# Performance work log

Measured on AMD Instinct MI355X. Metric: run time of the kernel, lower is better.

The kernel has to match this reference:

```python
import jax, jax.numpy as jnp
import numpy as np

NUM_HEADS = 4
EPS = 1e-5

def _proj(x, W, b):
    # 1x1x1 Conv3d == channel-wise linear: x [B,C,H,W,D], W [Cout,Cin], b [Cout]
    return jnp.einsum('oc,bchwd->bohwd', W, x) + b[None, :, None, None, None]

def setup_inputs() -> dict:
    key = jax.random.key(0)
    ks = jax.random.split(key, 12)
    B, C, H, W, D = 2, 128, 16, 16, 16
    s = 1.0 / np.sqrt(C)
    inp = {
        'query_features': jax.random.normal(ks[0], (B, C, H, W, D), jnp.float32),
        'key_value_features': jax.random.normal(ks[1], (B, C, H, W, D), jnp.float32),
        'Wq': jax.random.normal(ks[2], (C, C), jnp.float32) * s,
        'bq': jax.random.normal(ks[3], (C,), jnp.float32) * 0.01,
        'Wk': jax.random.normal(ks[4], (C, C), jnp.float32) * s,
        'bk': jax.random.normal(ks[5], (C,), jnp.float32) * 0.01,
        'Wv': jax.random.normal(ks[6], (C, C), jnp.float32) * s,
        'bv': jax.random.normal(ks[7], (C,), jnp.float32) * 0.01,
        'Wo': jax.random.normal(ks[8], (C, C), jnp.float32) * s,
        'bo': jax.random.normal(ks[9], (C,), jnp.float32) * 0.01,
    }
    return inp

def reference(query_features, key_value_features, Wq, bq, Wk, bk, Wv, bv, Wo, bo):
    B, C, H, W, D = query_features.shape
    hd = C // NUM_HEADS  # head_dim
    N = H * W * D
    Q = _proj(query_features, Wq, bq).reshape(B, NUM_HEADS, hd, N)
    K = _proj(key_value_features, Wk, bk).reshape(B, NUM_HEADS, hd, N)
    V = _proj(key_value_features, Wv, bv).reshape(B, NUM_HEADS, hd, N)
    scale = hd ** -0.5
    attn = jnp.einsum('bhdn,bhdm->bhnm', Q, K) * scale  # [B,h,N,N]
    attn = jax.nn.softmax(attn, axis=-1)
    out = jnp.einsum('bhnm,bhdm->bhdn', attn, V).reshape(B, C, H, W, D)
    out = _proj(out, Wo, bo)
    res = query_features + out
    # InstanceNorm3d (affine=False): normalize over spatial dims per (B,C)
    mu = jnp.mean(res, axis=(2, 3, 4), keepdims=True)
    var = jnp.var(res, axis=(2, 3, 4), keepdims=True)
    return (res - mu) * jax.lax.rsqrt(var + EPS)
```

## Files before the change

### kernel.cpp

```cpp
#include <hip/hip_runtime.h>
#include <hip/hip_bf16.h>

typedef unsigned short u16;
typedef unsigned int u32;
typedef __bf16 bf16_t;
typedef bf16_t bf16x8 __attribute__((ext_vector_type(8)));
typedef float f32x4 __attribute__((ext_vector_type(4)));

#define NTOT 4096
#define CCH 128
#define QSCL 0.25503486703f

__device__ __forceinline__ float bf2f(u16 x) {
    return __uint_as_float(((u32)x) << 16);
}
__device__ __forceinline__ u32 pkbf(float a, float b) {
    __hip_bfloat162 h = __float22bfloat162_rn(make_float2(a, b));
    u32 r; __builtin_memcpy(&r, &h, 4); return r;
}
__device__ __forceinline__ u16 f2bf(float a) {
    return (u16)(pkbf(a, a) & 0xffffu);
}

__global__ __launch_bounds__(256) void prep_kernel(
    const float* __restrict__ Wq, const float* __restrict__ Wk,
    const float* __restrict__ Wv, const float* __restrict__ Wo,
    const float* __restrict__ bq,
    u16* __restrict__ Wqb, u16* __restrict__ Wkb,
    u16* __restrict__ Wvb, u16* __restrict__ Wob,
    float* __restrict__ bqs)
{
    const int idx = blockIdx.x * 256 + threadIdx.x;
    const int m = idx >> 13;
    const int e = idx & 8191;
    const float* src = (m == 0) ? Wq : (m == 1) ? Wk : (m == 2) ? Wv : Wo;
    u32* dst = (u32*)((m == 0) ? Wqb : (m == 1) ? Wkb : (m == 2) ? Wvb : Wob);
    const float s = (m == 0) ? QSCL : 1.0f;
    float2 f = ((const float2*)src)[e];
    dst[e] = pkbf(f.x * s, f.y * s);
    if (idx < CCH) bqs[idx] = bq[idx] * QSCL;
}

__global__ __launch_bounds__(256, 4) void proj_kernel(
    const float* __restrict__ xq, const float* __restrict__ xkv,
    const u16* __restrict__ Wqb, const float* __restrict__ bqs,
    const u16* __restrict__ Wkb, const float* __restrict__ bk_,
    const u16* __restrict__ Wvb, const float* __restrict__ bv_,
    u16* __restrict__ Qt, u16* __restrict__ Kt, u16* __restrict__ Vn)
{
    const int nt = blockIdx.x, p = blockIdx.y, b = blockIdx.z;
    const float* X    = (p == 0) ? xq : xkv;
    const u16*   Wb   = (p == 0) ? Wqb : (p == 1) ? Wkb : Wvb;
    const float* bias = (p == 0) ? bqs : (p == 1) ? bk_ : bv_;
    const int n0 = nt * 64;
    const int tid = threadIdx.x;

    __shared__ u16 Xt[64 * 128];
    __shared__ u16 Wl[128 * 136];

    #pragma unroll
    for (int k = 0; k < 4; ++k) {
        int n = tid & 63;
        int c = (tid >> 6) + k * 4;
        float f[8];
        #pragma unroll
        for (int j = 0; j < 8; ++j)
            f[j] = X[((size_t)(b * CCH) + 8 * c + j) * NTOT + n0 + n];
        uint4 vv = {pkbf(f[0], f[1]), pkbf(f[2], f[3]), pkbf(f[4], f[5]), pkbf(f[6], f[7])};
        *(uint4*)(Xt + n * 128 + ((c ^ (n & 7)) * 8)) = vv;
    }
    #pragma unroll
    for (int k = 0; k < 8; ++k) {
        int id = tid + k * 256;
        int row = id >> 4;
        int off = (id & 15) * 8;
        *(uint4*)(Wl + row * 136 + off) = *(const uint4*)(Wb + row * 128 + off);
    }
    __syncthreads();

    const int wave = tid >> 6, lane = tid & 63;
    const int quad = lane >> 4, l16 = lane & 15;
    f32x4 acc[8];
    #pragma unroll
    for (int cf = 0; cf < 8; ++cf) acc[cf] = (f32x4){0.f, 0.f, 0.f, 0.f};

    #pragma unroll
    for (int kk = 0; kk < 4; ++kk) {
        bf16x8 bx = *(const bf16x8*)(Xt + (wave * 16 + l16) * 128 +
                                     (((kk * 4 + quad) ^ (l16 & 7)) * 8));
        #pragma unroll
        for (int cf = 0; cf < 8; ++cf) {
            bf16x8 aw = *(const bf16x8*)(Wl + (cf * 16 + l16) * 136 + kk * 32 + quad * 8);
            acc[cf] = __builtin_amdgcn_mfma_f32_16x16x32_bf16(aw, bx, acc[cf], 0, 0, 0);
        }
    }

    const int n = n0 + wave * 16 + l16;
    #pragma unroll
    for (int cf = 0; cf < 8; ++cf) {
        float4 b4 = *(const float4*)(bias + cf * 16 + quad * 4);
        float v0 = acc[cf][0] + b4.x;
        float v1 = acc[cf][1] + b4.y;
        float v2 = acc[cf][2] + b4.z;
        float v3 = acc[cf][3] + b4.w;
        if (p < 2) {
            const int h = cf >> 1;
            const int d0 = (cf & 1) * 16 + quad * 4;
            u16* dst = (p == 0 ? Qt : Kt) + ((size_t)(b * 4 + h) * NTOT + n) * 32 + d0;
            uint2 vv = {pkbf(v0, v1), pkbf(v2, v3)};
            *(uint2*)dst = vv;
        } else {
            int c = cf * 16 + quad * 4;
            u16* dst = Vn + (size_t)(b * CCH + c) * NTOT + n;
            dst[0 * NTOT] = f2bf(v0); dst[1 * NTOT] = f2bf(v1);
            dst[2 * NTOT] = f2bf(v2); dst[3 * NTOT] = f2bf(v3);
        }
    }
}

__global__ __launch_bounds__(256, 2) void flash_attn_kernel(
    const u16* __restrict__ Qt, const u16* __restrict__ Kt,
    const u16* __restrict__ Vn, u16* __restrict__ pO, float* __restrict__ pL)
{
    const int bh = blockIdx.z, kc = blockIdx.y;
    const int wave = threadIdx.x >> 6, lane = threadIdx.x & 63;
    const int q = lane >> 4, l16 = lane & 15;
    const int q0w = blockIdx.x * 256 + wave * 64;

    const u16* Qbh = Qt + (size_t)bh * NTOT * 32;
    const u16* Kbh = Kt + (size_t)bh * NTOT * 32;
    const u16* Vg  = Vn + ((size_t)((bh >> 2) * CCH + (bh & 3) * 32)) * NTOT;

    __shared__ u16 Kb[2][2048];
    __shared__ u16 Vb[2][2048];
    __shared__ u16 Pb[4][1024];

    const int kbase = kc * 1024;

    bf16x8 bq[4];
    #pragma unroll
    for (int g = 0; g < 4; ++g)
        bq[g] = *(const bf16x8*)(Qbh + (size_t)(q0w + g * 16 + l16) * 32 + q * 8);

    const size_t ksrc = (size_t)(wave * 16 + l16) * 32 + q * 8;
    const size_t vsrc = (size_t)((wave & 1) * 16 + l16) * NTOT + (wave >> 1) * 32 + q * 8;
    const int kv_dst = wave * 512 + lane * 8;

    uint4 kreg = *(const uint4*)(Kbh + (size_t)kbase * 32 + ksrc);
    uint4 vreg = *(const uint4*)(Vg + vsrc + kbase);
    *(uint4*)(&Kb[0][kv_dst]) = kreg;
    *(uint4*)(&Vb[0][kv_dst]) = vreg;
    __syncthreads();

    f32x4 o[4][2];
    #pragma unroll
    for (int g = 0; g < 4; ++g) {
        o[g][0] = (f32x4){0,0,0,0};
        o[g][1] = (f32x4){0,0,0,0};
    }
    const f32x4 zero = {0,0,0,0};
    float lp[4] = {0.f, 0.f, 0.f, 0.f};

    u16* pw = &Pb[wave][0];
    const int pwr = (q >> 1) * 128 + l16 * 8 + (q & 1) * 4;
    const int prd0 = 0 * 512 + lane * 8;
    const int prd1 = 1 * 512 + lane * 8;

    for (int it = 0; it < 16; ++it) {
        const int cur = it & 1;
        if (it < 15) {
            const int m1 = kbase + (it + 1) * 64;
            kreg = *(const uint4*)(Kbh + (size_t)m1 * 32 + ksrc);
            vreg = *(const uint4*)(Vg + vsrc + m1);
        }
        f32x4 s[4][4];
        #pragma unroll
        for (int t = 0; t < 4; ++t) {
            bf16x8 ak = *(const bf16x8*)(&Kb[cur][t * 512 + lane * 8]);
            #pragma unroll
            for (int g = 0; g < 4; ++g)
                s[g][t] = __builtin_amdgcn_mfma_f32_16x16x32_bf16(ak, bq[g], zero, 0, 0, 0);
        }
        bf16x8 av00 = *(const bf16x8*)(&Vb[cur][0 * 512 + lane * 8]);
        bf16x8 av01 = *(const bf16x8*)(&Vb[cur][1 * 512 + lane * 8]);
        bf16x8 av10 = *(const bf16x8*)(&Vb[cur][2 * 512 + lane * 8]);
        bf16x8 av11 = *(const bf16x8*)(&Vb[cur][3 * 512 + lane * 8]);
        #pragma unroll
        for (int g = 0; g < 4; ++g) {
            #pragma unroll
            for (int t = 0; t < 4; ++t) {
                float p0 = __builtin_amdgcn_exp2f(s[g][t][0]);
                float p1 = __builtin_amdgcn_exp2f(s[g][t][1]);
                float p2 = __builtin_amdgcn_exp2f(s[g][t][2]);
                float p3 = __builtin_amdgcn_exp2f(s[g][t][3]);
                lp[g] += (p0 + p1) + (p2 + p3);
                uint2 wv = {pkbf(p0, p1), pkbf(p2, p3)};
                *(uint2*)(pw + (t >> 1) * 512 + (t & 1) * 256 + pwr) = wv;
            }
            bf16x8 pb0 = *(const bf16x8*)(pw + prd0);
            bf16x8 pb1 = *(const bf16x8*)(pw + prd1);
            o[g][0] = __builtin_amdgcn_mfma_f32_16x16x32_bf16(av00, pb0, o[g][0], 0, 0, 0);
            o[g][1] = __builtin_amdgcn_mfma_f32_16x16x32_bf16(av01, pb0, o[g][1], 0, 0, 0);
            o[g][0] = __builtin_amdgcn_mfma_f32_16x16x32_bf16(av10, pb1, o[g][0], 0, 0, 0);
            o[g][1] = __builtin_amdgcn_mfma_f32_16x16x32_bf16(av11, pb1, o[g][1], 0, 0, 0);
        }
        if (it < 15) {
            const int nb = (it + 1) & 1;
            *(uint4*)(&Kb[nb][kv_dst]) = kreg;
            *(uint4*)(&Vb[nb][kv_dst]) = vreg;
        }
        __syncthreads();
    }

    #pragma unroll
    for (int g = 0; g < 4; ++g) {
        lp[g] += __shfl_xor(lp[g], 16);
        lp[g] += __shfl_xor(lp[g], 32);
        const size_t ob = ((size_t)(kc * 8 + bh) * NTOT + q0w + g * 16 + l16) * 32 + q * 4;
        uint2 w0 = {pkbf(o[g][0][0], o[g][0][1]), pkbf(o[g][0][2], o[g][0][3])};
        uint2 w1 = {pkbf(o[g][1][0], o[g][1][1]), pkbf(o[g][1][2], o[g][1][3])};
        *(uint2*)(pO + ob)      = w0;
        *(uint2*)(pO + ob + 16) = w1;
        if (q == 0)
            pL[(size_t)(kc * 8 + bh) * NTOT + q0w + g * 16 + l16] = lp[g];
    }
}

__global__ __launch_bounds__(256, 4) void outproj_kernel(
    const float* __restrict__ xq,
    const u16* __restrict__ pO, const float* __restrict__ pL,
    const u16* __restrict__ Wob, const float* __restrict__ bo,
    float* __restrict__ res, float* __restrict__ partS, float* __restrict__ partQ)
{
    const int nt = blockIdx.x, ct = blockIdx.y, b = blockIdx.z;
    const int n0 = nt * 64;
    const int tid = threadIdx.x;

    __shared__ u16 Xt[64 * 128];
    __shared__ u16 Wl[64 * 136];

    #pragma unroll
    for (int k = 0; k < 4; ++k) {
        int cid = tid + k * 256;
        int n = cid >> 4;
        int ch = cid & 15;
        int bh = b * 4 + (ch >> 2);
        int d0 = (ch & 3) * 8;
        float l = 0.f;
        float v[8];
        #pragma unroll
        for (int j = 0; j < 8; ++j) v[j] = 0.f;
        #pragma unroll
        for (int kcc = 0; kcc < 4; ++kcc) {
            const size_t nrow = (size_t)(kcc * 8 + bh) * NTOT + n0 + n;
            l += pL[nrow];
            uint4 u = *(const uint4*)(pO + nrow * 32 + d0);
            const u32 uu[4] = {u.x, u.y, u.z, u.w};
            #pragma unroll
            for (int j = 0; j < 4; ++j) {
                v[2 * j]     += bf2f((u16)(uu[j] & 0xffffu));
                v[2 * j + 1] += bf2f((u16)(uu[j] >> 16));
            }
        }
        const float inv = 1.0f / l;
        uint4 vv = {pkbf(v[0] * inv, v[1] * inv), pkbf(v[2] * inv, v[3] * inv),
                    pkbf(v[4] * inv, v[5] * inv), pkbf(v[6] * inv, v[7] * inv)};
        *(uint4*)(Xt + n * 128 + ((ch ^ (n & 7)) * 8)) = vv;
    }
    #pragma unroll
    for (int k = 0; k < 4; ++k) {
        int id = tid + k * 256;
        int row = id >> 4;
        int off = (id & 15) * 8;
        *(uint4*)(Wl + row * 136 + off) =
            *(const uint4*)(Wob + (size_t)(ct * 64 + row) * 128 + off);
    }
    __syncthreads();

    const int wave = tid >> 6, lane = tid & 63;
    const int quad = lane >> 4, l16 = lane & 15;
    f32x4 acc[4];
    #pragma unroll
    for (int cf = 0; cf < 4; ++cf) acc[cf] = (f32x4){0.f, 0.f, 0.f, 0.f};

    #pragma unroll
    for (int kk = 0; kk < 4; ++kk) {
        bf16x8 bx = *(const bf16x8*)(Xt + (wave * 16 + l16) * 128 +
                                     (((kk * 4 + quad) ^ (l16 & 7)) * 8));
        #pragma unroll
        for (int cf = 0; cf < 4; ++cf) {
            bf16x8 aw = *(const bf16x8*)(Wl + (cf * 16 + l16) * 136 + kk * 32 + quad * 8);
            acc[cf] = __builtin_amdgcn_mfma_f32_16x16x32_bf16(aw, bx, acc[cf], 0, 0, 0);
        }
    }

    const int n = n0 + wave * 16 + l16;
    const int tile = nt * 4 + wave;
    #pragma unroll
    for (int cf = 0; cf < 4; ++cf) {
        float4 b4 = *(const float4*)(bo + ct * 64 + cf * 16 + quad * 4);
        const float bb[4] = {b4.x, b4.y, b4.z, b4.w};
        float sv[4], qv[4];
        #pragma unroll
        for (int r = 0; r < 4; ++r) {
            int c = ct * 64 + cf * 16 + quad * 4 + r;
            float v = acc[cf][r] + bb[r] + xq[(size_t)(b * CCH + c) * NTOT + n];
            res[(size_t)(b * CCH + c) * NTOT + n] = v;
            sv[r] = v;
            qv[r] = v * v;
        }
        #pragma unroll
        for (int off = 1; off < 16; off <<= 1) {
            #pragma unroll
            for (int r = 0; r < 4; ++r) {
                sv[r] += __shfl_xor(sv[r], off);
                qv[r] += __shfl_xor(qv[r], off);
            }
        }
        if (l16 == 0) {
            #pragma unroll
            for (int r = 0; r < 4; ++r) {
                int c = ct * 64 + cf * 16 + quad * 4 + r;
                partS[(size_t)(b * CCH + c) * 256 + tile] = sv[r];
                partQ[(size_t)(b * CCH + c) * 256 + tile] = qv[r];
            }
        }
    }
}

__global__ __launch_bounds__(256) void norm_kernel(
    const float* __restrict__ res, const float* __restrict__ partS,
    const float* __restrict__ partQ, float* __restrict__ out)
{
    const int c = blockIdx.x, b = blockIdx.y;
    const int tid = threadIdx.x;
    const size_t row = (size_t)(b * CCH + c);
    __shared__ float rs[4], rq[4];
    float s = partS[row * 256 + tid];
    float q = partQ[row * 256 + tid];
    #pragma unroll
    for (int off = 1; off < 64; off <<= 1) {
        s += __shfl_xor(s, off);
        q += __shfl_xor(q, off);
    }
    const int wv = tid >> 6, ln = tid & 63;
    if (ln == 0) { rs[wv] = s; rq[wv] = q; }
    __syncthreads();
    float ts = rs[0] + rs[1] + rs[2] + rs[3];
    float tq = rq[0] + rq[1] + rq[2] + rq[3];
    float mu  = ts * (1.0f / 4096.0f);
    float var = tq * (1.0f / 4096.0f) - mu * mu;
    float inv = rsqrtf(var + 1e-5f);
    const size_t base = row * NTOT;
    #pragma unroll
    for (int j = 0; j < 4; ++j) {
        int n = tid * 4 + j * 1024;
        float4 v = *(const float4*)(res + base + n);
        float4 o;
        o.x = (v.x - mu) * inv; o.y = (v.y - mu) * inv;
        o.z = (v.z - mu) * inv; o.w = (v.w - mu) * inv;
        *(float4*)(out + base + n) = o;
    }
}

extern "C" void kernel_launch(void* const* d_in, const int* in_sizes, int n_in,
                              void* d_out, int out_size, void* d_ws, size_t ws_size,
                              hipStream_t stream)
{
    const float* xq  = (const float*)d_in[0];
    const float* xkv = (const float*)d_in[1];
    const float* Wq  = (const float*)d_in[2];
    const float* bq  = (const float*)d_in[3];
    const float* Wk  = (const float*)d_in[4];
    const float* bk  = (const float*)d_in[5];
    const float* Wv  = (const float*)d_in[6];
    const float* bv  = (const float*)d_in[7];
    const float* Wo  = (const float*)d_in[8];
    const float* bo  = (const float*)d_in[9];
    float* out = (float*)d_out;

    char* ws = (char*)d_ws;
    const size_t MB = (size_t)1 << 20;
    u16* Qt = (u16*)(ws + 0 * MB);
    u16* Kt = (u16*)(ws + 2 * MB);
    u16* Vn = (u16*)(ws + 4 * MB);
    u16* pO = (u16*)(ws + 6 * MB);
    float* pL = (float*)(ws + 14 * MB);
    u16* Wqb = (u16*)(ws + 15 * MB);
    u16* Wkb = Wqb + 16384;
    u16* Wvb = Wkb + 16384;
    u16* Wob = Wvb + 16384;
    float* bqs = (float*)(Wob + 16384);
    float* res   = (float*)(ws + 16 * MB);
    float* partS = (float*)(ws + 20 * MB);
    float* partQ = (float*)(ws + 20 * MB + 262144);

    prep_kernel<<<dim3(128), 256, 0, stream>>>(Wq, Wk, Wv, Wo, bq, Wqb, Wkb, Wvb, Wob, bqs);
    proj_kernel<<<dim3(64, 3, 2), 256, 0, stream>>>(xq, xkv, Wqb, bqs, Wkb, bk, Wvb, bv, Qt, Kt, Vn);
    flash_attn_kernel<<<dim3(16, 4, 8), 256, 0, stream>>>(Qt, Kt, Vn, pO, pL);
    outproj_kernel<<<dim3(64, 2, 2), 256, 0, stream>>>(xq, pO, pL, Wob, bo, res, partS, partQ);
    norm_kernel<<<dim3(128, 2), 256, 0, stream>>>(res, partS, partQ, out);
}
```

Measured before the change: 126.7 us.

## Fuse weight conversion into projections and double flash-attention key splits

```diff
diff --git a/kernel.cpp b/kernel.cpp
--- a/kernel.cpp
+++ b/kernel.cpp
@@ -22,36 +22,18 @@
     return (u16)(pkbf(a, a) & 0xffffu);
 }
 
-__global__ __launch_bounds__(256) void prep_kernel(
-    const float* __restrict__ Wq, const float* __restrict__ Wk,
-    const float* __restrict__ Wv, const float* __restrict__ Wo,
-    const float* __restrict__ bq,
-    u16* __restrict__ Wqb, u16* __restrict__ Wkb,
-    u16* __restrict__ Wvb, u16* __restrict__ Wob,
-    float* __restrict__ bqs)
-{
-    const int idx = blockIdx.x * 256 + threadIdx.x;
-    const int m = idx >> 13;
-    const int e = idx & 8191;
-    const float* src = (m == 0) ? Wq : (m == 1) ? Wk : (m == 2) ? Wv : Wo;
-    u32* dst = (u32*)((m == 0) ? Wqb : (m == 1) ? Wkb : (m == 2) ? Wvb : Wob);
-    const float s = (m == 0) ? QSCL : 1.0f;
-    float2 f = ((const float2*)src)[e];
-    dst[e] = pkbf(f.x * s, f.y * s);
-    if (idx < CCH) bqs[idx] = bq[idx] * QSCL;
-}
-
 __global__ __launch_bounds__(256, 4) void proj_kernel(
     const float* __restrict__ xq, const float* __restrict__ xkv,
-    const u16* __restrict__ Wqb, const float* __restrict__ bqs,
-    const u16* __restrict__ Wkb, const float* __restrict__ bk_,
-    const u16* __restrict__ Wvb, const float* __restrict__ bv_,
+    const float* __restrict__ Wq, const float* __restrict__ bq_,
+    const float* __restrict__ Wk, const float* __restrict__ bk_,
+    const float* __restrict__ Wv, const float* __restrict__ bv_,
     u16* __restrict__ Qt, u16* __restrict__ Kt, u16* __restrict__ Vn)
 {
     const int nt = blockIdx.x, p = blockIdx.y, b = blockIdx.z;
     const float* X    = (p == 0) ? xq : xkv;
-    const u16*   Wb   = (p == 0) ? Wqb : (p == 1) ? Wkb : Wvb;
-    const float* bias = (p == 0) ? bqs : (p == 1) ? bk_ : bv_;
+    const float* W    = (p == 0) ? Wq : (p == 1) ? Wk : Wv;
+    const float* bias = (p == 0) ? bq_ : (p == 1) ? bk_ : bv_;
+    const float scl   = (p == 0) ? QSCL : 1.0f;
     const int n0 = nt * 64;
     const int tid = threadIdx.x;
 
@@ -74,7 +56,12 @@
         int id = tid + k * 256;
         int row = id >> 4;
         int off = (id & 15) * 8;
-        *(uint4*)(Wl + row * 136 + off) = *(const uint4*)(Wb + row * 128 + off);
+        const float* wsrc = W + (size_t)row * 128 + off;
+        float4 f0 = *(const float4*)(wsrc);
+        float4 f1 = *(const float4*)(wsrc + 4);
+        uint4 vv = {pkbf(f0.x * scl, f0.y * scl), pkbf(f0.z * scl, f0.w * scl),
+                    pkbf(f1.x * scl, f1.y * scl), pkbf(f1.z * scl, f1.w * scl)};
+        *(uint4*)(Wl + row * 136 + off) = vv;
     }
     __syncthreads();
 
@@ -99,10 +86,10 @@
     #pragma unroll
     for (int cf = 0; cf < 8; ++cf) {
         float4 b4 = *(const float4*)(bias + cf * 16 + quad * 4);
-        float v0 = acc[cf][0] + b4.x;
-        float v1 = acc[cf][1] + b4.y;
-        float v2 = acc[cf][2] + b4.z;
-        float v3 = acc[cf][3] + b4.w;
+        float v0 = acc[cf][0] + b4.x * scl;
+        float v1 = acc[cf][1] + b4.y * scl;
+        float v2 = acc[cf][2] + b4.z * scl;
+        float v3 = acc[cf][3] + b4.w * scl;
         if (p < 2) {
             const int h = cf >> 1;
             const int d0 = (cf & 1) * 16 + quad * 4;
@@ -118,7 +105,7 @@
     }
 }
 
-__global__ __launch_bounds__(256, 2) void flash_attn_kernel(
+__global__ __launch_bounds__(256, 4) void flash_attn_kernel(
     const u16* __restrict__ Qt, const u16* __restrict__ Kt,
     const u16* __restrict__ Vn, u16* __restrict__ pO, float* __restrict__ pL)
 {
@@ -135,7 +122,7 @@
     __shared__ u16 Vb[2][2048];
     __shared__ u16 Pb[4][1024];
 
-    const int kbase = kc * 1024;
+    const int kbase = kc * 512;
 
     bf16x8 bq[4];
     #pragma unroll
@@ -166,9 +153,9 @@
     const int prd0 = 0 * 512 + lane * 8;
     const int prd1 = 1 * 512 + lane * 8;
 
-    for (int it = 0; it < 16; ++it) {
+    for (int it = 0; it < 8; ++it) {
         const int cur = it & 1;
-        if (it < 15) {
+        if (it < 7) {
             const int m1 = kbase + (it + 1) * 64;
             kreg = *(const uint4*)(Kbh + (size_t)m1 * 32 + ksrc);
             vreg = *(const uint4*)(Vg + vsrc + m1);
@@ -204,7 +191,7 @@
             o[g][0] = __builtin_amdgcn_mfma_f32_16x16x32_bf16(av10, pb1, o[g][0], 0, 0, 0);
             o[g][1] = __builtin_amdgcn_mfma_f32_16x16x32_bf16(av11, pb1, o[g][1], 0, 0, 0);
         }
-        if (it < 15) {
+        if (it < 7) {
             const int nb = (it + 1) & 1;
             *(uint4*)(&Kb[nb][kv_dst]) = kreg;
             *(uint4*)(&Vb[nb][kv_dst]) = vreg;
@@ -229,7 +216,7 @@
 __global__ __launch_bounds__(256, 4) void outproj_kernel(
     const float* __restrict__ xq,
     const u16* __restrict__ pO, const float* __restrict__ pL,
-    const u16* __restrict__ Wob, const float* __restrict__ bo,
+    const float* __restrict__ Wo, const float* __restrict__ bo,
     float* __restrict__ res, float* __restrict__ partS, float* __restrict__ partQ)
 {
     const int nt = blockIdx.x, ct = blockIdx.y, b = blockIdx.z;
@@ -251,7 +238,7 @@
         #pragma unroll
         for (int j = 0; j < 8; ++j) v[j] = 0.f;
         #pragma unroll
-        for (int kcc = 0; kcc < 4; ++kcc) {
+        for (int kcc = 0; kcc < 8; ++kcc) {
             const size_t nrow = (size_t)(kcc * 8 + bh) * NTOT + n0 + n;
             l += pL[nrow];
             uint4 u = *(const uint4*)(pO + nrow * 32 + d0);
@@ -272,8 +259,12 @@
         int id = tid + k * 256;
         int row = id >> 4;
         int off = (id & 15) * 8;
-        *(uint4*)(Wl + row * 136 + off) =
-            *(const uint4*)(Wob + (size_t)(ct * 64 + row) * 128 + off);
+        const float* wsrc = Wo + (size_t)(ct * 64 + row) * 128 + off;
+        float4 f0 = *(const float4*)(wsrc);
+        float4 f1 = *(const float4*)(wsrc + 4);
+        uint4 vv = {pkbf(f0.x, f0.y), pkbf(f0.z, f0.w),
+                    pkbf(f1.x, f1.y), pkbf(f1.z, f1.w)};
+        *(uint4*)(Wl + row * 136 + off) = vv;
     }
     __syncthreads();
 
@@ -385,19 +376,13 @@
     u16* Kt = (u16*)(ws + 2 * MB);
     u16* Vn = (u16*)(ws + 4 * MB);
     u16* pO = (u16*)(ws + 6 * MB);
-    float* pL = (float*)(ws + 14 * MB);
-    u16* Wqb = (u16*)(ws + 15 * MB);
-    u16* Wkb = Wqb + 16384;
-    u16* Wvb = Wkb + 16384;
-    u16* Wob = Wvb + 16384;
-    float* bqs = (float*)(Wob + 16384);
-    float* res   = (float*)(ws + 16 * MB);
-    float* partS = (float*)(ws + 20 * MB);
-    float* partQ = (float*)(ws + 20 * MB + 262144);
-
-    prep_kernel<<<dim3(128), 256, 0, stream>>>(Wq, Wk, Wv, Wo, bq, Wqb, Wkb, Wvb, Wob, bqs);
-    proj_kernel<<<dim3(64, 3, 2), 256, 0, stream>>>(xq, xkv, Wqb, bqs, Wkb, bk, Wvb, bv, Qt, Kt, Vn);
-    flash_attn_kernel<<<dim3(16, 4, 8), 256, 0, stream>>>(Qt, Kt, Vn, pO, pL);
-    outproj_kernel<<<dim3(64, 2, 2), 256, 0, stream>>>(xq, pO, pL, Wob, bo, res, partS, partQ);
+    float* pL = (float*)(ws + 22 * MB);
+    float* res   = (float*)(ws + 23 * MB);
+    float* partS = (float*)(ws + 27 * MB);
+    float* partQ = (float*)(ws + 27 * MB + 262144);
+
+    proj_kernel<<<dim3(64, 3, 2), 256, 0, stream>>>(xq, xkv, Wq, bq, Wk, bk, Wv, bv, Qt, Kt, Vn);
+    flash_attn_kernel<<<dim3(16, 8, 8), 256, 0, stream>>>(Qt, Kt, Vn, pO, pL);
+    outproj_kernel<<<dim3(64, 2, 2), 256, 0, stream>>>(xq, pO, pL, Wo, bo, res, partS, partQ);
     norm_kernel<<<dim3(128, 2), 256, 0, stream>>>(res, partS, partQ, out);
 }
```

Measured after the change: 161.0 us. 27.1% more time.
